# Kernel tuning notes

Hardware: AMD Instinct MI355X
Metric: run time of the kernel (lower is better)

## Reference

```python
import jax, jax.numpy as jnp
import numpy as np

# ---- config (mirrors CoInHead init + TARGET_ASSIGNER_CONFIG) ----
PCR0, PCR1 = -51.2, -51.2          # point_cloud_range x/y min
VX, VY = 0.05, 0.05                # voxel_size x/y
STRIDE = 4                         # FEATURE_MAP_STRIDE
FW, FH = 512, 512                  # feature_map_size [x, y] = grid/stride
NUM_CLASSES = 10
NUM_MAX_OBJS = 500
OVERLAP = 0.1                      # GAUSSIAN_OVERLAP
MIN_RADIUS = 2
RMAX = 16                          # static cap on radius (covers all synthetic boxes)
K = 2 * RMAX + 1                   # fixed gaussian patch size
EPS = float(np.finfo(np.float32).eps)
BATCH = 16


def _gaussian_radius(height, width, min_overlap):
    # faithful to centernet_utils.gaussian_radius (OpenPCDet)
    b1 = height + width
    c1 = width * height * (1.0 - min_overlap) / (1.0 + min_overlap)
    sq1 = jnp.sqrt(jnp.maximum(b1 * b1 - 4.0 * c1, 0.0))
    r1 = (b1 + sq1) / 2.0

    b2 = 2.0 * (height + width)
    c2 = (1.0 - min_overlap) * width * height
    sq2 = jnp.sqrt(jnp.maximum(b2 * b2 - 16.0 * c2, 0.0))
    r2 = (b2 + sq2) / 2.0

    a3 = 4.0 * min_overlap
    b3 = -2.0 * min_overlap * (height + width)
    c3 = (min_overlap - 1.0) * width * height
    sq3 = jnp.sqrt(jnp.maximum(b3 * b3 - 4.0 * a3 * c3, 0.0))
    r3 = (b3 + sq3) / (2.0 * a3)
    return jnp.minimum(jnp.minimum(r1, r2), r3)


def setup_inputs() -> dict:
    key = jax.random.key(0)
    ks = jax.random.split(key, 8)
    B, M = BATCH, NUM_MAX_OBJS
    x = jax.random.uniform(ks[0], (B, M), minval=-50.0, maxval=50.0)
    y = jax.random.uniform(ks[1], (B, M), minval=-50.0, maxval=50.0)
    z = jax.random.uniform(ks[2], (B, M), minval=-2.0, maxval=1.0)
    dx = jax.random.uniform(ks[3], (B, M), minval=0.5, maxval=6.0)
    dy = jax.random.uniform(ks[4], (B, M), minval=0.5, maxval=6.0)
    dz = jax.random.uniform(ks[5], (B, M), minval=0.5, maxval=3.0)
    heading = jax.random.uniform(ks[6], (B, M), minval=-np.pi, maxval=np.pi)
    cls = jax.random.randint(ks[7], (B, M), 1, NUM_CLASSES + 1).astype(jnp.float32)
    gt_boxes = jnp.stack([x, y, z, dx, dy, dz, heading, cls], axis=-1).astype(jnp.float32)
    return {"gt_boxes": gt_boxes}


def reference(gt_boxes):
    # vectorized assign_target_of_single_head over (batch, objects)
    B, M, _ = gt_boxes.shape
    f32 = jnp.float32
    x, y, z = gt_boxes[..., 0], gt_boxes[..., 1], gt_boxes[..., 2]
    dx, dy, dz = gt_boxes[..., 3], gt_boxes[..., 4], gt_boxes[..., 5]
    heading = gt_boxes[..., 6]
    cls = (gt_boxes[..., 7] - 1.0).astype(jnp.int32)          # 0-based class id

    coord_x = jnp.clip((x - PCR0) / VX / STRIDE, 0.0, FW - 0.5)
    coord_y = jnp.clip((y - PCR1) / VY / STRIDE, 0.0, FH - 0.5)
    cxi = coord_x.astype(jnp.int32)
    cyi = coord_y.astype(jnp.int32)

    dxf = dx / VX / STRIDE
    dyf = dy / VY / STRIDE
    radius = _gaussian_radius(dxf, dyf, OVERLAP)
    radius = jnp.clip(radius.astype(jnp.int32), MIN_RADIUS, RMAX)  # (B, M)

    valid = (dxf > 0) & (dyf > 0) & (cxi >= 0) & (cxi <= FW) & (cyi >= 0) & (cyi <= FH)

    # fixed KxK gaussian patch centered on the integer center
    off = jnp.arange(K, dtype=jnp.int32) - RMAX
    oi = off[:, None]                                   # (K,1) row offset
    oj = off[None, :]                                   # (1,K) col offset
    sigma = (2.0 * radius.astype(f32) + 1.0) / 6.0      # diameter/6
    d2 = (oi * oi + oj * oj).astype(f32)                # (K,K)
    g = jnp.exp(-d2[None, None] / (2.0 * sigma[..., None, None] ** 2))  # (B,M,K,K)
    g = jnp.where(g < EPS, 0.0, g)                      # gaussian_2d eps truncation

    r_bm = radius[..., None, None]
    within = (jnp.abs(oi)[None, None] <= r_bm) & (jnp.abs(oj)[None, None] <= r_bm)
    yy = cyi[..., None, None] + oi[None, None]          # (B,M,K,K)
    xx = cxi[..., None, None] + oj[None, None]
    inb = (yy >= 0) & (yy < FH) & (xx >= 0) & (xx < FW)
    vals = jnp.where(valid[..., None, None] & within & inb, g, 0.0)

    b_idx = jnp.arange(B, dtype=jnp.int32)[:, None, None, None]
    c_idx = jnp.clip(cls, 0, NUM_CLASSES - 1)[..., None, None]
    heatmap = jnp.zeros((B, NUM_CLASSES, FH, FW), f32).at[
        b_idx, c_idx, jnp.clip(yy, 0, FH - 1), jnp.clip(xx, 0, FW - 1)
    ].max(vals)

    inds = jnp.where(valid, cyi * FW + cxi, 0).astype(jnp.int64)
    mask = valid.astype(jnp.int64)

    vf = valid.astype(f32)[..., None]
    ret_boxes = jnp.stack([
        coord_x - cxi.astype(f32),
        coord_y - cyi.astype(f32),
        z,
        jnp.log(jnp.maximum(dx, 1e-12)),
        jnp.log(jnp.maximum(dy, 1e-12)),
        jnp.log(jnp.maximum(dz, 1e-12)),
        jnp.cos(heading),
        jnp.sin(heading),
    ], axis=-1) * vf                                     # (B,M,8)

    return heatmap, ret_boxes, inds, mask
```

## Files before the change

kernel.cpp:

```cpp
#include <hip/hip_runtime.h>
#include <hip/hip_bf16.h>

#define PCR0   (-51.2f)
#define PCR1   (-51.2f)
#define VX_    (0.05f)
#define VY_    (0.05f)
#define STRIDE_ 4.0f
#define FW_    512
#define FH_    512
#define NCLS   10
#define NOBJ   500
#define OVERLAP_ 0.1f
#define MINRAD 2
#define RMAX_  16
#define BATCH_ 16
#define EPS_   1.1920928955078125e-07f

#define HEATMAP_ELEMS  (BATCH_ * NCLS * FH_ * FW_)
#define RETBOX_OFF     HEATMAP_ELEMS
#define RETBOX_ELEMS   (BATCH_ * NOBJ * 8)
#define INDS_OFF       (RETBOX_OFF + RETBOX_ELEMS)
#define MASK_OFF       (INDS_OFF + BATCH_ * NOBJ)

#define TILE_  32
#define TPB_   (FW_ / TILE_)
#define NTILES (TPB_ * TPB_)
#define CAP_   512

#define CNT_BYTES   (BATCH_ * NTILES * 4)
#define REC_OFF     CNT_BYTES
#define REC_BYTES   (BATCH_ * NOBJ * 32)
#define LIST_OFF    (REC_OFF + REC_BYTES)
#define LIST_BYTES  ((size_t)BATCH_ * NTILES * CAP_ * 4)
#define WS_NEEDED   (LIST_OFF + LIST_BYTES)

struct __align__(16) ObjRec {
    int   cxi, cyi, rad, cls;
    float negInv;
    int   valid;
    float pad0, pad1;
};

__device__ __forceinline__ void obj_params(const float* g8,
        float& coord_x, float& coord_y, int& cxi, int& cyi,
        int& radius, bool& valid)
{
    const float x = g8[0], y = g8[1];
    const float dx = g8[3], dy = g8[4];

    coord_x = fminf(fmaxf((x - PCR0) / VX_ / STRIDE_, 0.f), (float)FW_ - 0.5f);
    coord_y = fminf(fmaxf((y - PCR1) / VY_ / STRIDE_, 0.f), (float)FH_ - 0.5f);
    cxi = (int)coord_x;
    cyi = (int)coord_y;

    float dxf = dx / VX_ / STRIDE_;
    float dyf = dy / VY_ / STRIDE_;

    const float h = dxf, w = dyf, o = OVERLAP_;
    float b1 = h + w;
    float c1 = w * h * (1.f - o) / (1.f + o);
    float r1 = (b1 + sqrtf(fmaxf(b1 * b1 - 4.f * c1, 0.f))) * 0.5f;
    float b2 = 2.f * (h + w);
    float c2 = (1.f - o) * w * h;
    float r2 = (b2 + sqrtf(fmaxf(b2 * b2 - 16.f * c2, 0.f))) * 0.5f;
    float a3 = 4.f * o;
    float b3 = -2.f * o * (h + w);
    float c3 = (o - 1.f) * w * h;
    float r3 = (b3 + sqrtf(fmaxf(b3 * b3 - 4.f * a3 * c3, 0.f))) / (2.f * a3);
    float radf = fminf(fminf(r1, r2), r3);
    radius = (int)radf;
    radius = min(max(radius, MINRAD), RMAX_);

    valid = (dxf > 0.f) && (dyf > 0.f) &&
            (cxi >= 0) && (cxi <= FW_) && (cyi >= 0) && (cyi <= FH_);
}

__global__ void phaseA(const float* __restrict__ gt, float* __restrict__ out,
                       int* __restrict__ cnt, int* __restrict__ lists,
                       ObjRec* __restrict__ recs)
{
    int obj = blockIdx.x * blockDim.x + threadIdx.x;
    if (obj >= BATCH_ * NOBJ) return;
    int b = obj / NOBJ;

    const float* g8 = gt + (size_t)obj * 8;
    float coord_x, coord_y; int cxi, cyi, radius; bool valid;
    obj_params(g8, coord_x, coord_y, cxi, cyi, radius, valid);

    const float z = g8[2], dx = g8[3], dy = g8[4], dz = g8[5];
    const float hd = g8[6], clsf = g8[7];

    float vf = valid ? 1.f : 0.f;
    float* rb = out + RETBOX_OFF + (size_t)obj * 8;
    rb[0] = (coord_x - (float)cxi) * vf;
    rb[1] = (coord_y - (float)cyi) * vf;
    rb[2] = z * vf;
    rb[3] = logf(fmaxf(dx, 1e-12f)) * vf;
    rb[4] = logf(fmaxf(dy, 1e-12f)) * vf;
    rb[5] = logf(fmaxf(dz, 1e-12f)) * vf;
    rb[6] = cosf(hd) * vf;
    rb[7] = sinf(hd) * vf;
    out[INDS_OFF + obj] = valid ? (float)(cyi * FW_ + cxi) : 0.f;
    out[MASK_OFF + obj] = vf;

    int c = min(max((int)(clsf - 1.0f), 0), NCLS - 1);
    float sigma = (2.f * (float)radius + 1.f) / 6.f;
    float denom = 2.f * sigma * sigma;

    ObjRec r;
    r.cxi = cxi; r.cyi = cyi; r.rad = radius; r.cls = c;
    r.negInv = -1.0f / denom;
    r.valid = valid ? 1 : 0;
    r.pad0 = 0.f; r.pad1 = 0.f;
    recs[obj] = r;

    if (!valid) return;

    int tx0 = max(cxi - radius, 0) >> 5;
    int tx1 = min(cxi + radius, FW_ - 1) >> 5;
    int ty0 = max(cyi - radius, 0) >> 5;
    int ty1 = min(cyi + radius, FH_ - 1) >> 5;
    for (int ty = ty0; ty <= ty1; ++ty) {
        for (int tx = tx0; tx <= tx1; ++tx) {
            int bin = b * NTILES + ty * TPB_ + tx;
            int pos = atomicAdd(&cnt[bin], 1);
            if (pos < CAP_) lists[(size_t)bin * CAP_ + pos] = obj;
        }
    }
}

__global__ __launch_bounds__(256) void phaseB(
        float* __restrict__ out,
        const int* __restrict__ cnt, const int* __restrict__ lists,
        const ObjRec* __restrict__ recs)
{
    int bid  = blockIdx.x;
    int b    = bid >> 8;
    int tile = bid & (NTILES - 1);
    int ty = tile >> 4, tx = tile & (TPB_ - 1);

    int lr  = threadIdx.x >> 3;
    int lc  = (threadIdx.x & 7) << 2;
    int py  = (ty << 5) + lr;
    int px0 = (tx << 5) + lc;

    float acc[NCLS][4];
    #pragma unroll
    for (int c = 0; c < NCLS; ++c) {
        acc[c][0] = 0.f; acc[c][1] = 0.f; acc[c][2] = 0.f; acc[c][3] = 0.f;
    }

    int bin = b * NTILES + tile;
    int n = cnt[bin]; if (n > CAP_) n = CAP_;
    const int* lst = lists + (size_t)bin * CAP_;

    for (int k2 = 0; k2 < n; ++k2) {
        int o = lst[k2];
        ObjRec r = recs[o];
        int rad = r.rad;
        int ry = py - r.cyi;
        bool rowin = (ry >= -rad) && (ry <= rad);
        float fy = (float)(ry * ry);

        float val[4];
        #pragma unroll
        for (int k = 0; k < 4; ++k) {
            int rx = px0 + k - r.cxi;
            bool in = rowin && (rx >= -rad) && (rx <= rad);
            float d2 = fy + (float)(rx * rx);
            float g = expf(d2 * r.negInv);
            val[k] = (in && g >= EPS_) ? g : 0.f;
        }

        int cu = __builtin_amdgcn_readfirstlane(r.cls);
        #pragma unroll
        for (int c = 0; c < NCLS; ++c) {
            if (c == cu) {
                #pragma unroll
                for (int k = 0; k < 4; ++k)
                    acc[c][k] = fmaxf(acc[c][k], val[k]);
            }
        }
    }

    size_t plane = (size_t)FH_ * FW_;
    size_t base  = (size_t)b * NCLS * plane + (size_t)py * FW_ + px0;
    #pragma unroll
    for (int c = 0; c < NCLS; ++c) {
        float4 v = make_float4(acc[c][0], acc[c][1], acc[c][2], acc[c][3]);
        *(float4*)(out + base + (size_t)c * plane) = v;
    }
}

__global__ void zero_heatmap(float4* __restrict__ hm4, int n4) {
    int idx = blockIdx.x * blockDim.x + threadIdx.x;
    int stride = gridDim.x * blockDim.x;
    float4 z = make_float4(0.f, 0.f, 0.f, 0.f);
    for (int i = idx; i < n4; i += stride) hm4[i] = z;
}

__global__ __launch_bounds__(256) void paint_objects(
        const float* __restrict__ gt, float* __restrict__ out)
{
    const int obj = blockIdx.x;
    const int b   = obj / NOBJ;
    const float* g8 = gt + (size_t)obj * 8;

    float coord_x, coord_y; int cxi, cyi, radius; bool valid;
    obj_params(g8, coord_x, coord_y, cxi, cyi, radius, valid);

    const float z = g8[2], dx = g8[3], dy = g8[4], dz = g8[5];
    const float hd = g8[6], clsf = g8[7];

    if (threadIdx.x == 0) {
        float vf = valid ? 1.f : 0.f;
        float* rb = out + RETBOX_OFF + (size_t)obj * 8;
        rb[0] = (coord_x - (float)cxi) * vf;
        rb[1] = (coord_y - (float)cyi) * vf;
        rb[2] = z * vf;
        rb[3] = logf(fmaxf(dx, 1e-12f)) * vf;
        rb[4] = logf(fmaxf(dy, 1e-12f)) * vf;
        rb[5] = logf(fmaxf(dz, 1e-12f)) * vf;
        rb[6] = cosf(hd) * vf;
        rb[7] = sinf(hd) * vf;
        out[INDS_OFF + obj] = valid ? (float)(cyi * FW_ + cxi) : 0.f;
        out[MASK_OFF + obj] = vf;
    }
    if (!valid) return;

    float sigma = (2.f * (float)radius + 1.f) / 6.f;
    float denom = 2.f * sigma * sigma;
    int side = 2 * radius + 1;
    int npos = side * side;
    int c = min(max((int)(clsf - 1.0f), 0), NCLS - 1);
    float* hm = out + ((size_t)b * NCLS + c) * (size_t)(FH_ * FW_);

    for (int idx = threadIdx.x; idx < npos; idx += blockDim.x) {
        int i = idx / side - radius;
        int j = idx % side - radius;
        float d2 = (float)(i * i + j * j);
        float gv = expf(-d2 / denom);
        if (gv < EPS_) continue;
        int yy = cyi + i;
        int xx = cxi + j;
        if (yy < 0 || yy >= FH_ || xx < 0 || xx >= FW_) continue;
        atomicMax((int*)(hm + (size_t)yy * FW_ + xx), __float_as_int(gv));
    }
}

extern "C" void kernel_launch(void* const* d_in, const int* in_sizes, int n_in,
                              void* d_out, int out_size, void* d_ws, size_t ws_size,
                              hipStream_t stream) {
    const float* gt = (const float*)d_in[0];
    float* out = (float*)d_out;

    if (ws_size >= WS_NEEDED) {
        int* cnt      = (int*)d_ws;
        ObjRec* recs  = (ObjRec*)((char*)d_ws + REC_OFF);
        int* lists    = (int*)((char*)d_ws + LIST_OFF);

        hipMemsetAsync(cnt, 0, CNT_BYTES, stream);

        phaseA<<<(BATCH_ * NOBJ + 255) / 256, 256, 0, stream>>>(gt, out, cnt, lists, recs);
        phaseB<<<BATCH_ * NTILES, 256, 0, stream>>>(out, cnt, lists, recs);
    } else {
        int n4 = HEATMAP_ELEMS / 4;
        zero_heatmap<<<4096, 256, 0, stream>>>((float4*)out, n4);
        paint_objects<<<BATCH_ * NOBJ, 256, 0, stream>>>(gt, out);
    }
}
```

Measured before the change: 173.8 us.

## Bin objects per (batch, class, row band) and use separable gaussian in heatmap kernel

```diff
diff --git a/kernel.cpp b/kernel.cpp
--- a/kernel.cpp
+++ b/kernel.cpp
@@ -22,24 +22,17 @@
 #define INDS_OFF       (RETBOX_OFF + RETBOX_ELEMS)
 #define MASK_OFF       (INDS_OFF + BATCH_ * NOBJ)
 
-#define TILE_  32
-#define TPB_   (FW_ / TILE_)
-#define NTILES (TPB_ * TPB_)
-#define CAP_   512
-
-#define CNT_BYTES   (BATCH_ * NTILES * 4)
+#define BAND_  32
+#define NBAND  (FH_ / BAND_)
+#define NBINS  (BATCH_ * NCLS * NBAND)
+#define CAPB   NOBJ
+
+#define CNT_BYTES   (NBINS * 4)
 #define REC_OFF     CNT_BYTES
-#define REC_BYTES   (BATCH_ * NOBJ * 32)
+#define REC_BYTES   (BATCH_ * NOBJ * 16)
 #define LIST_OFF    (REC_OFF + REC_BYTES)
-#define LIST_BYTES  ((size_t)BATCH_ * NTILES * CAP_ * 4)
+#define LIST_BYTES  ((size_t)NBINS * CAPB * 4)
 #define WS_NEEDED   (LIST_OFF + LIST_BYTES)
-
-struct __align__(16) ObjRec {
-    int   cxi, cyi, rad, cls;
-    float negInv;
-    int   valid;
-    float pad0, pad1;
-};
 
 __device__ __forceinline__ void obj_params(const float* g8,
         float& coord_x, float& coord_y, int& cxi, int& cyi,
@@ -77,7 +70,7 @@
 
 __global__ void phaseA(const float* __restrict__ gt, float* __restrict__ out,
                        int* __restrict__ cnt, int* __restrict__ lists,
-                       ObjRec* __restrict__ recs)
+                       int4* __restrict__ recs)
 {
     int obj = blockIdx.x * blockDim.x + threadIdx.x;
     if (obj >= BATCH_ * NOBJ) return;
@@ -105,91 +98,81 @@
 
     int c = min(max((int)(clsf - 1.0f), 0), NCLS - 1);
     float sigma = (2.f * (float)radius + 1.f) / 6.f;
-    float denom = 2.f * sigma * sigma;
-
-    ObjRec r;
-    r.cxi = cxi; r.cyi = cyi; r.rad = radius; r.cls = c;
-    r.negInv = -1.0f / denom;
-    r.valid = valid ? 1 : 0;
-    r.pad0 = 0.f; r.pad1 = 0.f;
+    float negInv = -1.0f / (2.f * sigma * sigma);
+
+    int4 r;
+    r.x = cxi; r.y = cyi; r.z = radius; r.w = __float_as_int(negInv);
     recs[obj] = r;
 
     if (!valid) return;
 
-    int tx0 = max(cxi - radius, 0) >> 5;
-    int tx1 = min(cxi + radius, FW_ - 1) >> 5;
     int ty0 = max(cyi - radius, 0) >> 5;
     int ty1 = min(cyi + radius, FH_ - 1) >> 5;
+    int binbase = (b * NCLS + c) * NBAND;
     for (int ty = ty0; ty <= ty1; ++ty) {
-        for (int tx = tx0; tx <= tx1; ++tx) {
-            int bin = b * NTILES + ty * TPB_ + tx;
-            int pos = atomicAdd(&cnt[bin], 1);
-            if (pos < CAP_) lists[(size_t)bin * CAP_ + pos] = obj;
-        }
-    }
-}
-
-__global__ __launch_bounds__(256) void phaseB(
+        int bin = binbase + ty;
+        int pos = atomicAdd(&cnt[bin], 1);
+        if (pos < CAPB) lists[(size_t)bin * CAPB + pos] = obj;
+    }
+}
+
+__global__ __launch_bounds__(512) void phaseB(
         float* __restrict__ out,
         const int* __restrict__ cnt, const int* __restrict__ lists,
-        const ObjRec* __restrict__ recs)
-{
-    int bid  = blockIdx.x;
-    int b    = bid >> 8;
-    int tile = bid & (NTILES - 1);
-    int ty = tile >> 4, tx = tile & (TPB_ - 1);
-
-    int lr  = threadIdx.x >> 3;
-    int lc  = (threadIdx.x & 7) << 2;
-    int py  = (ty << 5) + lr;
-    int px0 = (tx << 5) + lc;
-
-    float acc[NCLS][4];
+        const int4* __restrict__ recs)
+{
+    const int bid = blockIdx.x;
+    const int t   = threadIdx.x;
+    const int col0  = (t & 127) << 2;
+    const int r0    = __builtin_amdgcn_readfirstlane(t >> 7);
+    const int wbase = __builtin_amdgcn_readfirstlane(((t >> 6) & 1) << 8);
+    const int y0    = (bid & (NBAND - 1)) << 5;
+
+    float acc[8][4];
     #pragma unroll
-    for (int c = 0; c < NCLS; ++c) {
-        acc[c][0] = 0.f; acc[c][1] = 0.f; acc[c][2] = 0.f; acc[c][3] = 0.f;
-    }
-
-    int bin = b * NTILES + tile;
-    int n = cnt[bin]; if (n > CAP_) n = CAP_;
-    const int* lst = lists + (size_t)bin * CAP_;
-
-    for (int k2 = 0; k2 < n; ++k2) {
-        int o = lst[k2];
-        ObjRec r = recs[o];
-        int rad = r.rad;
-        int ry = py - r.cyi;
-        bool rowin = (ry >= -rad) && (ry <= rad);
-        float fy = (float)(ry * ry);
-
-        float val[4];
+    for (int s = 0; s < 8; ++s) {
+        acc[s][0] = 0.f; acc[s][1] = 0.f; acc[s][2] = 0.f; acc[s][3] = 0.f;
+    }
+
+    int n = cnt[bid]; if (n > CAPB) n = CAPB;
+    const int* lst = lists + (size_t)bid * CAPB;
+
+    for (int it = 0; it < n; ++it) {
+        int o = __builtin_amdgcn_readfirstlane(lst[it]);
+        int4 r = recs[o];
+        int cxi   = __builtin_amdgcn_readfirstlane(r.x);
+        int cyi   = __builtin_amdgcn_readfirstlane(r.y);
+        int rad   = __builtin_amdgcn_readfirstlane(r.z);
+        float negInv = __int_as_float(__builtin_amdgcn_readfirstlane(r.w));
+
+        if (cxi + rad < wbase || cxi - rad > wbase + 255) continue;
+
+        float cexp[4]; bool colin[4];
         #pragma unroll
         for (int k = 0; k < 4; ++k) {
-            int rx = px0 + k - r.cxi;
-            bool in = rowin && (rx >= -rad) && (rx <= rad);
-            float d2 = fy + (float)(rx * rx);
-            float g = expf(d2 * r.negInv);
-            val[k] = (in && g >= EPS_) ? g : 0.f;
+            int rx = col0 + k - cxi;
+            colin[k] = (rx >= -rad) && (rx <= rad);
+            cexp[k]  = __expf((float)(rx * rx) * negInv);
         }
 
-        int cu = __builtin_amdgcn_readfirstlane(r.cls);
         #pragma unroll
-        for (int c = 0; c < NCLS; ++c) {
-            if (c == cu) {
-                #pragma unroll
-                for (int k = 0; k < 4; ++k)
-                    acc[c][k] = fmaxf(acc[c][k], val[k]);
+        for (int s = 0; s < 8; ++s) {
+            int ry = y0 + 4 * s + r0 - cyi;
+            if (ry < -rad || ry > rad) continue;
+            float rexp = __expf((float)(ry * ry) * negInv);
+            #pragma unroll
+            for (int k = 0; k < 4; ++k) {
+                float g = rexp * cexp[k];
+                bool ok = colin[k] && (g >= EPS_);
+                acc[s][k] = ok ? fmaxf(acc[s][k], g) : acc[s][k];
             }
         }
     }
 
-    size_t plane = (size_t)FH_ * FW_;
-    size_t base  = (size_t)b * NCLS * plane + (size_t)py * FW_ + px0;
+    float4* out4 = (float4*)(out + (size_t)bid * (BAND_ * FW_));
     #pragma unroll
-    for (int c = 0; c < NCLS; ++c) {
-        float4 v = make_float4(acc[c][0], acc[c][1], acc[c][2], acc[c][3]);
-        *(float4*)(out + base + (size_t)c * plane) = v;
-    }
+    for (int s = 0; s < 8; ++s)
+        out4[s * 512 + t] = make_float4(acc[s][0], acc[s][1], acc[s][2], acc[s][3]);
 }
 
 __global__ void zero_heatmap(float4* __restrict__ hm4, int n4) {
@@ -255,14 +238,14 @@
     float* out = (float*)d_out;
 
     if (ws_size >= WS_NEEDED) {
-        int* cnt      = (int*)d_ws;
-        ObjRec* recs  = (ObjRec*)((char*)d_ws + REC_OFF);
-        int* lists    = (int*)((char*)d_ws + LIST_OFF);
+        int* cnt     = (int*)d_ws;
+        int4* recs   = (int4*)((char*)d_ws + REC_OFF);
+        int* lists   = (int*)((char*)d_ws + LIST_OFF);
 
         hipMemsetAsync(cnt, 0, CNT_BYTES, stream);
 
         phaseA<<<(BATCH_ * NOBJ + 255) / 256, 256, 0, stream>>>(gt, out, cnt, lists, recs);
-        phaseB<<<BATCH_ * NTILES, 256, 0, stream>>>(out, cnt, lists, recs);
+        phaseB<<<NBINS, 512, 0, stream>>>(out, cnt, lists, recs);
     } else {
         int n4 = HEATMAP_ELEMS / 4;
         zero_heatmap<<<4096, 256, 0, stream>>>((float4*)out, n4);
```

Result: no change. 170.7 us (-1.8%).
